# Optimization experiments

Hardware: AMD Instinct MI355X
Metric: run time of the kernel (lower is better)

## Reference

```python
import jax, jax.numpy as jnp
import numpy as np

B, H, Wd = 32, 64, 64
C_IN = 65            # ambient Lorentz dim (1 time + 64 space)
KH = KW = 3          # kernel
OUT = 256            # out_channels (ambient); linear space dim = 255
HCAT = (C_IN - 1) * KH * KW + 1  # 577
CURV = 1.0


def setup_inputs() -> dict:
    key = jax.random.key(0)
    k1, k2, k3 = jax.random.split(key, 3)
    # spatial (tangent-like) components, projected onto the hyperboloid
    v = jax.random.normal(k1, (B, H, Wd, C_IN - 1), dtype=jnp.float32) * 0.5
    t = jnp.sqrt(1.0 / CURV + jnp.sum(v * v, axis=-1, keepdims=True))
    x = jnp.concatenate([t, v], axis=-1)  # valid Lorentz points, (B,H,W,65)
    W = jax.random.normal(k2, (OUT - 1, HCAT), dtype=jnp.float32) * (1.0 / np.sqrt(HCAT))
    b = jnp.zeros((OUT - 1,), dtype=jnp.float32)
    return {"x": x, "W": W, "b": b}


def reference(x, W, b):
    c = CURV
    Bn, Hn, Wn, C = x.shape
    # 'SAME' padding with stride 1, kernel 3 -> pad 1 on each side, edge mode
    xp = jnp.pad(x, ((0, 0), (1, 1), (1, 1), (0, 0)), mode="edge")
    # im2col: stack the KH*KW shifted views -> (B, H, W, N, C)
    slabs = [xp[:, i:i + Hn, j:j + Wn, :] for i in range(KH) for j in range(KW)]
    patches = jnp.stack(slabs, axis=3)
    N = KH * KW
    # Lorentz direct concatenation (HCat):
    # time = sqrt(sum_i t_i^2 - (N-1)/c), space = concat of spatial parts
    t_cat = jnp.sqrt(jnp.sum(patches[..., 0] ** 2, axis=-1) - (N - 1) / c)
    sp = patches[..., 1:].reshape(Bn, Hn, Wn, N * (C - 1))
    h = jnp.concatenate([t_cat[..., None], sp], axis=-1)  # (B,H,W,577)
    # Hyperbolic linear (Lorentz fully-connected): space part is affine map,
    # time part restores the Lorentz constraint <y,y>_L = -1/c
    z = jnp.einsum("bhwi,oi->bhwo", h, W) + b  # (B,H,W,255)
    t_out = jnp.sqrt(1.0 / c + jnp.sum(z * z, axis=-1, keepdims=True))
    return jnp.concatenate([t_out, z], axis=-1)  # (B,H,W,256)
```

## Files before the change

### kernel.cpp

```cpp
#include <hip/hip_runtime.h>
#include <hip/hip_bf16.h>


#define CLAMP63(v) ((v) < 0 ? 0 : ((v) > 63 ? 63 : (v)))

typedef __attribute__((ext_vector_type(8))) short short8;
typedef __attribute__((ext_vector_type(4))) float floatx4;

__device__ __forceinline__ void gl2lds16(const void* g, void* l) {
  __builtin_amdgcn_global_load_lds(
      (const __attribute__((address_space(1))) void*)g,
      (__attribute__((address_space(3))) void*)l, 16, 0, 0);
}

__global__ void prep_x(const float* __restrict__ x, __hip_bfloat16* __restrict__ xs,
                       float* __restrict__ tsq) {
  int idx = blockIdx.x * 256 + threadIdx.x;
  int p = idx >> 6, c = idx & 63;
  xs[idx] = __float2bfloat16(x[p * 65 + 1 + c]);
  if (c == 0) { float t = x[p * 65]; tsq[p] = t * t; }
}

__global__ void prep_tcat(const float* __restrict__ tsq, float* __restrict__ tcat) {
  int p = blockIdx.x * 256 + threadIdx.x;
  int xx = p & 63, yy = (p >> 6) & 63, bb = p >> 12;
  float s = 0.f;
#pragma unroll
  for (int dy = -1; dy <= 1; ++dy) {
    int y2 = CLAMP63(yy + dy);
#pragma unroll
    for (int dx = -1; dx <= 1; ++dx) {
      int x2 = CLAMP63(xx + dx);
      s += tsq[(bb * 64 + y2) * 64 + x2];
    }
  }
  tcat[p] = sqrtf(s - 8.0f);
}

__global__ void prep_w(const float* __restrict__ W, const float* __restrict__ b,
                       __hip_bfloat16* __restrict__ Wb, float* __restrict__ Wt0,
                       float* __restrict__ bp) {
  int n = blockIdx.x;
  for (int k = threadIdx.x; k < 576; k += 256) {
    float v = (n < 255) ? W[n * 577 + 1 + k] : 0.f;
    Wb[n * 576 + k] = __float2bfloat16(v);
  }
  if (threadIdx.x == 0) {
    Wt0[n] = (n < 255) ? W[n * 577] : 0.f;
    bp[n] = (n < 255) ? b[n] : 0.f;
  }
}

__launch_bounds__(256, 2)
__global__ void hypconv_main(const __hip_bfloat16* __restrict__ xs,
                             const __hip_bfloat16* __restrict__ Wb,
                             const float* __restrict__ Wt0,
                             const float* __restrict__ bp,
                             const float* __restrict__ tcat,
                             float* __restrict__ out) {
  __shared__ ushort Ab[128 * 32];
  __shared__ ushort Bb[256 * 32];
  __shared__ float sq_lds[256];

  const int tid = threadIdx.x;
  const int w = tid >> 6;
  const int lane = tid & 63;
  const int quad = lane >> 4;
  const int ln = lane & 15;
  const int pix_base = blockIdx.x * 128;

  int a_kg[2], a_bx[2], a_by[2], a_bb[2];
#pragma unroll
  for (int q = 0; q < 2; ++q) {
    int i = (w * 2 + q) * 64 + lane;
    a_kg[q] = i & 3;
    int pix = pix_base + (i >> 2);
    a_bx[q] = pix & 63; a_by[q] = (pix >> 6) & 63; a_bb[q] = pix >> 12;
  }
  int b_n[4], b_kg[4];
#pragma unroll
  for (int p = 0; p < 4; ++p) {
    int i = (w * 4 + p) * 64 + lane;
    b_n[p] = i >> 2; b_kg[p] = i & 3;
  }

  const int m_off = (w >> 1) * 64;
  const int n_off = (w & 1) * 128;

  floatx4 acc[4][8];
#pragma unroll
  for (int mf = 0; mf < 4; ++mf)
#pragma unroll
    for (int nf = 0; nf < 8; ++nf)
      acc[mf][nf] = (floatx4){0.f, 0.f, 0.f, 0.f};

  for (int it = 0; it < 18; ++it) {
    __syncthreads();
    const int nbr = it >> 1;
    const int dy = nbr / 3 - 1, dx = nbr % 3 - 1;
    const int c0 = (it & 1) * 32;
#pragma unroll
    for (int q = 0; q < 2; ++q) {
      int y2 = CLAMP63(a_by[q] + dy);
      int x2 = CLAMP63(a_bx[q] + dx);
      const __hip_bfloat16* src =
          xs + (size_t)((a_bb[q] * 64 + y2) * 64 + x2) * 64 + c0 + a_kg[q] * 8;
      gl2lds16(src, &Ab[(w * 2 + q) * 512]);
    }
#pragma unroll
    for (int p = 0; p < 4; ++p) {
      const __hip_bfloat16* src = Wb + b_n[p] * 576 + it * 32 + b_kg[p] * 8;
      gl2lds16(src, &Bb[(w * 4 + p) * 512]);
    }
    __syncthreads();

    short8 af[4], bfr[8];
#pragma unroll
    for (int mf = 0; mf < 4; ++mf)
      af[mf] = *(const short8*)&Ab[(m_off + mf * 16 + ln) * 32 + quad * 8];
#pragma unroll
    for (int nf = 0; nf < 8; ++nf)
      bfr[nf] = *(const short8*)&Bb[(n_off + nf * 16 + ln) * 32 + quad * 8];
#pragma unroll
    for (int mf = 0; mf < 4; ++mf)
#pragma unroll
      for (int nf = 0; nf < 8; ++nf)
        acc[mf][nf] = __builtin_amdgcn_mfma_f32_16x16x32_bf16(af[mf], bfr[nf], acc[mf][nf], 0, 0, 0);
  }

  float wn[8], bnv[8];
#pragma unroll
  for (int nf = 0; nf < 8; ++nf) {
    int n = n_off + nf * 16 + ln;
    wn[nf] = Wt0[n];
    bnv[nf] = bp[n];
  }
  float tc[4][4];
#pragma unroll
  for (int mf = 0; mf < 4; ++mf)
#pragma unroll
    for (int r = 0; r < 4; ++r)
      tc[mf][r] = tcat[pix_base + m_off + mf * 16 + quad * 4 + r];

  float sq[4][4];
#pragma unroll
  for (int mf = 0; mf < 4; ++mf) {
#pragma unroll
    for (int r = 0; r < 4; ++r) {
      int m = m_off + mf * 16 + quad * 4 + r;
      size_t orow = (size_t)(pix_base + m) * 256;
      float s = 0.f;
#pragma unroll
      for (int nf = 0; nf < 8; ++nf) {
        int n = n_off + nf * 16 + ln;
        float z = acc[mf][nf][r] + bnv[nf] + tc[mf][r] * wn[nf];
        s += z * z;
        if (n < 255) out[orow + 1 + n] = z;
      }
      sq[mf][r] = s;
    }
  }

#pragma unroll
  for (int mf = 0; mf < 4; ++mf)
#pragma unroll
    for (int r = 0; r < 4; ++r) {
      float s = sq[mf][r];
      s += __shfl_xor(s, 1, 64);
      s += __shfl_xor(s, 2, 64);
      s += __shfl_xor(s, 4, 64);
      s += __shfl_xor(s, 8, 64);
      if (ln == 0)
        sq_lds[(w & 1) * 128 + m_off + mf * 16 + quad * 4 + r] = s;
    }
  __syncthreads();
  if (tid < 128) {
    float s = sq_lds[tid] + sq_lds[128 + tid];
    out[(size_t)(pix_base + tid) * 256] = sqrtf(1.0f + s);
  }
}

extern "C" void kernel_launch(void* const* d_in, const int* in_sizes, int n_in,
                              void* d_out, int out_size, void* d_ws, size_t ws_size,
                              hipStream_t stream) {
  const float* x = (const float*)d_in[0];
  const float* W = (const float*)d_in[1];
  const float* b = (const float*)d_in[2];
  float* out = (float*)d_out;
  char* ws = (char*)d_ws;

  __hip_bfloat16* xs  = (__hip_bfloat16*)(ws);
  __hip_bfloat16* Wb  = (__hip_bfloat16*)(ws + 16777216);
  float*          Wt0 = (float*)(ws + 17072128);
  float*          bp  = (float*)(ws + 17073152);
  float*          tsq = (float*)(ws + 17074176);
  float*          tcat= (float*)(ws + 17598464);

  prep_x   <<<32768, 256, 0, stream>>>(x, xs, tsq);
  prep_w   <<<256,   256, 0, stream>>>(W, b, Wb, Wt0, bp);
  prep_tcat<<<512,   256, 0, stream>>>(tsq, tcat);
  hypconv_main<<<1024, 256, 0, stream>>>(xs, Wb, Wt0, bp, tcat, out);
}
```

Measured before the change: 226.9 us.

## Double-buffer GEMM loads, fuse tcat into main, coalesce output via LDS

The main GEMM loop now double-buffers the A and B tiles in LDS, so the next stage's global-to-LDS loads are issued before the current stage's MFMAs and one barrier per iteration is dropped. The LDS layout is reorganised into k-group-major order. The tcat computation moves into the main kernel, reading the time components straight from x, which removes the tsq/tcat buffers and one launch. prep_x is vectorised to convert 8 channels per thread. The epilogue stages z through LDS so each row is written with coalesced float4 stores and the time component is reduced per row. The costs are more LDS per block (48 KB), which may limit occupancy, plus extra barriers in the epilogue.

```diff
diff --git a/kernel.cpp b/kernel.cpp
--- a/kernel.cpp
+++ b/kernel.cpp
@@ -13,79 +13,75 @@
       (__attribute__((address_space(3))) void*)l, 16, 0, 0);
 }
 
-__global__ void prep_x(const float* __restrict__ x, __hip_bfloat16* __restrict__ xs,
-                       float* __restrict__ tsq) {
+__global__ void prep_x(const float* __restrict__ x, __hip_bfloat16* __restrict__ xs) {
   int idx = blockIdx.x * 256 + threadIdx.x;
-  int p = idx >> 6, c = idx & 63;
-  xs[idx] = __float2bfloat16(x[p * 65 + 1 + c]);
-  if (c == 0) { float t = x[p * 65]; tsq[p] = t * t; }
-}
-
-__global__ void prep_tcat(const float* __restrict__ tsq, float* __restrict__ tcat) {
-  int p = blockIdx.x * 256 + threadIdx.x;
-  int xx = p & 63, yy = (p >> 6) & 63, bb = p >> 12;
-  float s = 0.f;
+  int p = idx >> 3, g = idx & 7;
+  const float* src = x + (size_t)p * 65 + 1 + g * 8;
+  __align__(16) __hip_bfloat16 tmp[8];
 #pragma unroll
-  for (int dy = -1; dy <= 1; ++dy) {
-    int y2 = CLAMP63(yy + dy);
-#pragma unroll
-    for (int dx = -1; dx <= 1; ++dx) {
-      int x2 = CLAMP63(xx + dx);
-      s += tsq[(bb * 64 + y2) * 64 + x2];
-    }
-  }
-  tcat[p] = sqrtf(s - 8.0f);
+  for (int i = 0; i < 8; ++i) tmp[i] = __float2bfloat16(src[i]);
+  *(short8*)(xs + (size_t)idx * 8) = *(const short8*)tmp;
 }
 
 __global__ void prep_w(const float* __restrict__ W, const float* __restrict__ b,
                        __hip_bfloat16* __restrict__ Wb, float* __restrict__ Wt0,
                        float* __restrict__ bp) {
   int n = blockIdx.x;
-  for (int k = threadIdx.x; k < 576; k += 256) {
-    float v = (n < 255) ? W[n * 577 + 1 + k] : 0.f;
-    Wb[n * 576 + k] = __float2bfloat16(v);
-  }
+  for (int k = threadIdx.x; k < 576; k += 256)
+    Wb[n * 576 + k] = __float2bfloat16((n < 255) ? W[n * 577 + 1 + k] : 0.f);
   if (threadIdx.x == 0) {
     Wt0[n] = (n < 255) ? W[n * 577] : 0.f;
-    bp[n] = (n < 255) ? b[n] : 0.f;
+    bp[n]  = (n < 255) ? b[n] : 0.f;
   }
 }
 
+#define STAGE(IT, BUF)                                                          \
+  do {                                                                          \
+    const int nbr_ = (IT) >> 1;                                                 \
+    const int dy_ = nbr_ / 3 - 1, dx_ = nbr_ % 3 - 1;                           \
+    const int c0_ = ((IT) & 1) * 32;                                            \
+    _Pragma("unroll")                                                           \
+    for (int q = 0; q < 2; ++q) {                                               \
+      int y2 = CLAMP63(a_by[q] + dy_);                                          \
+      int x2 = CLAMP63(a_bx[q] + dx_);                                          \
+      const __hip_bfloat16* src =                                               \
+          xs + (size_t)((a_bb[q] * 64 + y2) * 64 + x2) * 64 + c0_ + w * 8;      \
+      gl2lds16(src, Ab + (BUF) * 4096 + (w * 2 + q) * 512);                     \
+    }                                                                           \
+    _Pragma("unroll")                                                           \
+    for (int p = 0; p < 4; ++p)                                                 \
+      gl2lds16(b_src[p] + (IT) * 32, Bb + (BUF) * 8192 + (w * 4 + p) * 512);    \
+  } while (0)
+
 __launch_bounds__(256, 2)
-__global__ void hypconv_main(const __hip_bfloat16* __restrict__ xs,
+__global__ void hypconv_main(const float* __restrict__ x,
+                             const __hip_bfloat16* __restrict__ xs,
                              const __hip_bfloat16* __restrict__ Wb,
                              const float* __restrict__ Wt0,
                              const float* __restrict__ bp,
-                             const float* __restrict__ tcat,
                              float* __restrict__ out) {
-  __shared__ ushort Ab[128 * 32];
-  __shared__ ushort Bb[256 * 32];
-  __shared__ float sq_lds[256];
+  __shared__ __align__(16) char smem[49152];
+  __shared__ float tc_lds[128];
+  ushort* Ab = (ushort*)smem;
+  ushort* Bb = (ushort*)(smem + 16384);
+  float* zbuf = (float*)smem;
 
   const int tid = threadIdx.x;
-  const int w = tid >> 6;
-  const int lane = tid & 63;
-  const int quad = lane >> 4;
-  const int ln = lane & 15;
+  const int w = tid >> 6, lane = tid & 63;
+  const int quad = lane >> 4, ln = lane & 15;
   const int pix_base = blockIdx.x * 128;
+  const int m_off = (w >> 1) * 64, n_off = (w & 1) * 128;
 
-  int a_kg[2], a_bx[2], a_by[2], a_bb[2];
+  int a_bx[2], a_by[2], a_bb[2];
 #pragma unroll
   for (int q = 0; q < 2; ++q) {
-    int i = (w * 2 + q) * 64 + lane;
-    a_kg[q] = i & 3;
-    int pix = pix_base + (i >> 2);
+    int pix = pix_base + q * 64 + lane;
     a_bx[q] = pix & 63; a_by[q] = (pix >> 6) & 63; a_bb[q] = pix >> 12;
   }
-  int b_n[4], b_kg[4];
+  const __hip_bfloat16* b_src[4];
 #pragma unroll
-  for (int p = 0; p < 4; ++p) {
-    int i = (w * 4 + p) * 64 + lane;
-    b_n[p] = i >> 2; b_kg[p] = i & 3;
-  }
-
-  const int m_off = (w >> 1) * 64;
-  const int n_off = (w & 1) * 128;
+  for (int p = 0; p < 4; ++p)
+    b_src[p] = Wb + (size_t)(p * 64 + lane) * 576 + w * 8;
 
   floatx4 acc[4][8];
 #pragma unroll
@@ -94,33 +90,37 @@
     for (int nf = 0; nf < 8; ++nf)
       acc[mf][nf] = (floatx4){0.f, 0.f, 0.f, 0.f};
 
+  STAGE(0, 0);
+
+  if (tid < 128) {
+    int pix = pix_base + tid;
+    int bx = pix & 63, by = (pix >> 6) & 63, bb = pix >> 12;
+    float s = 0.f;
+#pragma unroll
+    for (int dy = -1; dy <= 1; ++dy) {
+      int y2 = CLAMP63(by + dy);
+#pragma unroll
+      for (int dx = -1; dx <= 1; ++dx) {
+        int x2 = CLAMP63(bx + dx);
+        float t = x[(size_t)((bb * 64 + y2) * 64 + x2) * 65];
+        s += t * t;
+      }
+    }
+    tc_lds[tid] = sqrtf(s - 8.0f);
+  }
+
   for (int it = 0; it < 18; ++it) {
     __syncthreads();
-    const int nbr = it >> 1;
-    const int dy = nbr / 3 - 1, dx = nbr % 3 - 1;
-    const int c0 = (it & 1) * 32;
-#pragma unroll
-    for (int q = 0; q < 2; ++q) {
-      int y2 = CLAMP63(a_by[q] + dy);
-      int x2 = CLAMP63(a_bx[q] + dx);
-      const __hip_bfloat16* src =
-          xs + (size_t)((a_bb[q] * 64 + y2) * 64 + x2) * 64 + c0 + a_kg[q] * 8;
-      gl2lds16(src, &Ab[(w * 2 + q) * 512]);
-    }
-#pragma unroll
-    for (int p = 0; p < 4; ++p) {
-      const __hip_bfloat16* src = Wb + b_n[p] * 576 + it * 32 + b_kg[p] * 8;
-      gl2lds16(src, &Bb[(w * 4 + p) * 512]);
-    }
-    __syncthreads();
-
+    if (it < 17) STAGE(it + 1, (it + 1) & 1);
+    const ushort* Ar = Ab + (it & 1) * 4096;
+    const ushort* Br = Bb + (it & 1) * 8192;
     short8 af[4], bfr[8];
 #pragma unroll
     for (int mf = 0; mf < 4; ++mf)
-      af[mf] = *(const short8*)&Ab[(m_off + mf * 16 + ln) * 32 + quad * 8];
+      af[mf] = *(const short8*)&Ar[(quad * 128 + m_off + mf * 16 + ln) * 8];
 #pragma unroll
     for (int nf = 0; nf < 8; ++nf)
-      bfr[nf] = *(const short8*)&Bb[(n_off + nf * 16 + ln) * 32 + quad * 8];
+      bfr[nf] = *(const short8*)&Br[(quad * 256 + n_off + nf * 16 + ln) * 8];
 #pragma unroll
     for (int mf = 0; mf < 4; ++mf)
 #pragma unroll
@@ -128,6 +128,7 @@
         acc[mf][nf] = __builtin_amdgcn_mfma_f32_16x16x32_bf16(af[mf], bfr[nf], acc[mf][nf], 0, 0, 0);
   }
 
+  __syncthreads();
   float wn[8], bnv[8];
 #pragma unroll
   for (int nf = 0; nf < 8; ++nf) {
@@ -135,48 +136,37 @@
     wn[nf] = Wt0[n];
     bnv[nf] = bp[n];
   }
-  float tc[4][4];
-#pragma unroll
-  for (int mf = 0; mf < 4; ++mf)
-#pragma unroll
-    for (int r = 0; r < 4; ++r)
-      tc[mf][r] = tcat[pix_base + m_off + mf * 16 + quad * 4 + r];
 
-  float sq[4][4];
 #pragma unroll
   for (int mf = 0; mf < 4; ++mf) {
 #pragma unroll
     for (int r = 0; r < 4; ++r) {
-      int m = m_off + mf * 16 + quad * 4 + r;
-      size_t orow = (size_t)(pix_base + m) * 256;
-      float s = 0.f;
+      float tcv = tc_lds[m_off + mf * 16 + quad * 4 + r];
+      int lr = (w >> 1) * 16 + quad * 4 + r;
 #pragma unroll
       for (int nf = 0; nf < 8; ++nf) {
-        int n = n_off + nf * 16 + ln;
-        float z = acc[mf][nf][r] + bnv[nf] + tc[mf][r] * wn[nf];
-        s += z * z;
-        if (n < 255) out[orow + 1 + n] = z;
+        float z = acc[mf][nf][r] + bnv[nf] + tcv * wn[nf];
+        zbuf[lr * 256 + ((1 + n_off + nf * 16 + ln) & 255)] = z;
       }
-      sq[mf][r] = s;
     }
-  }
-
+    __syncthreads();
 #pragma unroll
-  for (int mf = 0; mf < 4; ++mf)
-#pragma unroll
-    for (int r = 0; r < 4; ++r) {
-      float s = sq[mf][r];
-      s += __shfl_xor(s, 1, 64);
-      s += __shfl_xor(s, 2, 64);
-      s += __shfl_xor(s, 4, 64);
-      s += __shfl_xor(s, 8, 64);
-      if (ln == 0)
-        sq_lds[(w & 1) * 128 + m_off + mf * 16 + quad * 4 + r] = s;
+    for (int rr = 0; rr < 8; ++rr) {
+      int lr = w * 8 + rr;
+      float4 v = *(const float4*)&zbuf[lr * 256 + lane * 4];
+      float ss = v.x * v.x + v.y * v.y + v.z * v.z + v.w * v.w;
+      ss += __shfl_xor(ss, 1, 64);
+      ss += __shfl_xor(ss, 2, 64);
+      ss += __shfl_xor(ss, 4, 64);
+      ss += __shfl_xor(ss, 8, 64);
+      ss += __shfl_xor(ss, 16, 64);
+      ss += __shfl_xor(ss, 32, 64);
+      float tout = sqrtf(1.0f + ss);
+      if (lane == 0) v.x = tout;
+      int m = (lr >> 4) * 64 + mf * 16 + (lr & 15);
+      *(float4*)&out[(size_t)(pix_base + m) * 256 + lane * 4] = v;
     }
-  __syncthreads();
-  if (tid < 128) {
-    float s = sq_lds[tid] + sq_lds[128 + tid];
-    out[(size_t)(pix_base + tid) * 256] = sqrtf(1.0f + s);
+    if (mf < 3) __syncthreads();
   }
 }
 
@@ -193,11 +183,8 @@
   __hip_bfloat16* Wb  = (__hip_bfloat16*)(ws + 16777216);
   float*          Wt0 = (float*)(ws + 17072128);
   float*          bp  = (float*)(ws + 17073152);
-  float*          tsq = (float*)(ws + 17074176);
-  float*          tcat= (float*)(ws + 17598464);
 
-  prep_x   <<<32768, 256, 0, stream>>>(x, xs, tsq);
-  prep_w   <<<256,   256, 0, stream>>>(W, b, Wb, Wt0, bp);
-  prep_tcat<<<512,   256, 0, stream>>>(tsq, tcat);
-  hypconv_main<<<1024, 256, 0, stream>>>(xs, Wb, Wt0, bp, tcat, out);
+  prep_x<<<4096, 256, 0, stream>>>(x, xs);
+  prep_w<<<256,  256, 0, stream>>>(W, b, Wb, Wt0, bp);
+  hypconv_main<<<1024, 256, 0, stream>>>(x, xs, Wb, Wt0, bp, out);
 }
```

After: 224.8 us. Within noise of the previous version (-0.9%).
